# Kernel optimization log

Hardware: AMD Instinct MI355X
Metric: run time of the kernel (lower is better)

Reference implementation:

```python
import jax, jax.numpy as jnp
import numpy as np

N, E, DIN, DOUT = 10000, 160000, 256, 256
NEG_SLOPE = 0.2
BN_EPS = 1e-5
DROP_P = 0.5


def setup_inputs() -> dict:
    key = jax.random.key(0)
    ks = jax.random.split(key, 12)
    s = 1.0 / np.sqrt(DIN)
    return {
        "x": jax.random.normal(ks[0], (N, DIN), jnp.float32),
        "edge_index": jax.random.randint(ks[1], (2, E), 0, N, jnp.int64),
        "Wl": jax.random.normal(ks[2], (DIN, DOUT), jnp.float32) * s,
        "bl": jax.random.normal(ks[3], (DOUT,), jnp.float32) * s,
        "Wr": jax.random.normal(ks[4], (DIN, DOUT), jnp.float32) * s,
        "br": jax.random.normal(ks[5], (DOUT,), jnp.float32) * s,
        "att": jax.random.normal(ks[6], (DOUT,), jnp.float32) * (1.0 / np.sqrt(DOUT)),
        "bias": jax.random.normal(ks[7], (DOUT,), jnp.float32) * 0.01,
        "gamma": jnp.ones((DOUT,), jnp.float32),
        "beta": jnp.zeros((DOUT,), jnp.float32),
        "dropout_u": jax.random.uniform(ks[8], (N, DOUT), jnp.float32),
    }


def reference(x, edge_index, Wl, bl, Wr, br, att, bias, gamma, beta, dropout_u):
    n = x.shape[0]
    # GATv2Conv (heads=1): separate source/target linear maps
    xl = x @ Wl + bl  # source features [N, DOUT]
    xr = x @ Wr + br  # target features [N, DOUT]
    # add self-loops (PyG default add_self_loops=True)
    loop = jnp.arange(n, dtype=edge_index.dtype)
    src = jnp.concatenate([edge_index[0], loop])  # [E+N]
    dst = jnp.concatenate([edge_index[1], loop])
    # GATv2 attention: e = att . LeakyReLU(xl_j + xr_i)
    h = jax.nn.leaky_relu(xl[src] + xr[dst], NEG_SLOPE)  # [E+N, DOUT]
    alpha = h @ att  # [E+N]
    # segment softmax over destination nodes
    amax = jax.ops.segment_max(alpha, dst, num_segments=n)
    alpha = jnp.exp(alpha - amax[dst])
    denom = jax.ops.segment_sum(alpha, dst, num_segments=n)
    alpha = alpha / denom[dst]
    # scatter-add aggregate of weighted source features
    out = jax.ops.segment_sum(xl[src] * alpha[:, None], dst, num_segments=n)
    out = out + bias
    # ReLU -> dropout(p=0.5, training) -> BatchNorm (training stats)
    out = jax.nn.relu(out)
    mask = (dropout_u >= DROP_P).astype(out.dtype) / (1.0 - DROP_P)
    out = out * mask
    mean = out.mean(axis=0)
    var = out.var(axis=0)  # biased, as BatchNorm uses for normalization
    out = gamma * (out - mean) * jax.lax.rsqrt(var + BN_EPS) + beta
    return out
```

## Files before the change

kernel.cpp:

```cpp
#include <hip/hip_runtime.h>
#include <hip/hip_bf16.h>
#include <math.h>

#define D 256
#define CAP 128
#define NEG_SLOPE 0.2f
#define BN_EPS 1e-5f
#define NBKT 64

typedef __attribute__((ext_vector_type(8))) short bf16x8;
typedef __attribute__((ext_vector_type(8))) unsigned short ushort8;
typedef __attribute__((ext_vector_type(4))) unsigned short ushort4v;
typedef __attribute__((ext_vector_type(4))) float f32x4;

__device__ inline unsigned short f2bf(float f) {
    union { float f; unsigned u; } v; v.f = f;
    unsigned u = v.u;
    unsigned r = u + 0x7FFFu + ((u >> 16) & 1u);
    return (unsigned short)(r >> 16);
}
__device__ inline float bf2f(unsigned short u) {
    union { unsigned u; float f; } v; v.u = ((unsigned)u) << 16; return v.f;
}

__device__ __forceinline__ void gload16(const void* g, void* l) {
    __builtin_amdgcn_global_load_lds(
        (const __attribute__((address_space(1))) unsigned int*)g,
        (__attribute__((address_space(3))) unsigned int*)l,
        16, 0, 0);
}

__global__ void prep_kernel(const float* __restrict__ X,
                            const float* __restrict__ Wl, const float* __restrict__ Wr,
                            int* __restrict__ zero_base, int nzero, int nzb,
                            unsigned short* __restrict__ Bt,
                            unsigned short* __restrict__ Xbf, int N) {
    int b = blockIdx.x;
    if (b < nzb) {
        int idx = b * 256 + threadIdx.x;
        if (idx < nzero) zero_base[idx] = 0;
    } else if (b < nzb + 128) {
        __shared__ float tile[32][33];
        int b2 = b - nzb;
        const float* W = (b2 < 64) ? Wl : Wr;
        int nbase = (b2 < 64) ? 0 : 256;
        int t2 = b2 & 63;
        int ti = t2 >> 3;
        int tj = t2 & 7;
        int t = threadIdx.x;
        int r = t >> 3;
        int c4 = (t & 7) * 4;
        float4 v = *(const float4*)(W + (size_t)(ti * 32 + r) * 256 + tj * 32 + c4);
        tile[r][c4] = v.x; tile[r][c4 + 1] = v.y;
        tile[r][c4 + 2] = v.z; tile[r][c4 + 3] = v.w;
        __syncthreads();
        int nl = t >> 3;
        int n = tj * 32 + nl;
        int k0 = ti * 32 + c4;
        int ks = k0 ^ ((n & 7) << 3);
        ushort4v o;
        o[0] = f2bf(tile[c4][nl]);
        o[1] = f2bf(tile[c4 + 1][nl]);
        o[2] = f2bf(tile[c4 + 2][nl]);
        o[3] = f2bf(tile[c4 + 3][nl]);
        *(ushort4v*)(Bt + (size_t)(nbase + n) * 256 + ks) = o;
    } else {
        int idx = (b - nzb - 128) * 256 + threadIdx.x;
        int row = idx >> 5;
        int k0 = (idx & 31) * 8;
        int ks = k0 ^ ((row & 7) << 3);
        ushort8 v = {0, 0, 0, 0, 0, 0, 0, 0};
        if (row < N) {
            const float* src = X + (size_t)row * 256 + k0;
            float4 f0 = *(const float4*)(src);
            float4 f1 = *(const float4*)(src + 4);
            v[0] = f2bf(f0.x); v[1] = f2bf(f0.y);
            v[2] = f2bf(f0.z); v[3] = f2bf(f0.w);
            v[4] = f2bf(f1.x); v[5] = f2bf(f1.y);
            v[6] = f2bf(f1.z); v[7] = f2bf(f1.w);
        }
        *(ushort8*)(Xbf + (size_t)row * 256 + ks) = v;
    }
}

__global__ __launch_bounds__(256) void gemm_scatter_kernel(
    const unsigned short* __restrict__ Xbf, const unsigned short* __restrict__ Bt,
    const float* __restrict__ bl, const float* __restrict__ br,
    const int* __restrict__ ei, int* __restrict__ counts, int* __restrict__ ssrc,
    unsigned short* __restrict__ xlbf, unsigned short* __restrict__ xrbf,
    int M, int E, int N, int ngemm, int nMtiles)
{
    if ((int)blockIdx.x >= ngemm) {
        int e = (blockIdx.x - ngemm) * 256 + threadIdx.x;
        if (e < E + N) {
            int src, dst;
            if (e < E) { src = ei[e]; dst = ei[E + e]; }
            else       { src = dst = e - E; }
            int pos = atomicAdd(&counts[dst], 1);
            if (pos < CAP) ssrc[dst * CAP + pos] = src;
        }
        return;
    }

    const int b = blockIdx.x;
    const int r = (b & 7) + 8 * (b >> 6);
    const int c = (b >> 3) & 7;
    if (r >= nMtiles) return;

    __shared__ __align__(16) unsigned short As[64 * 128];
    __shared__ __align__(16) unsigned short Bs[64 * 128];

    const int tid = threadIdx.x;
    const int wave = tid >> 6, lane = tid & 63;
    const int m_l = lane & 15, quad = lane >> 4;
    const int row0 = r * 64;
    const int n0 = c * 64;
    const int sw = (m_l & 7) << 3;

    f32x4 acc[4] = {};

    for (int k0 = 0; k0 < 256; k0 += 128) {
        __syncthreads();
        #pragma unroll
        for (int i = 0; i < 4; i++) {
            int L = (tid + i * 256) * 16;
            int rr = L >> 8;
            int cb = L & 255;
            gload16((const char*)Xbf + (size_t)(row0 + rr) * 512 + (size_t)k0 * 2 + cb,
                    (char*)As + L);
            gload16((const char*)Bt + (size_t)(n0 + rr) * 512 + (size_t)k0 * 2 + cb,
                    (char*)Bs + L);
        }
        __syncthreads();

        #pragma unroll
        for (int kk0 = 0; kk0 < 128; kk0 += 32) {
            int ka = (kk0 + quad * 8) ^ sw;
            bf16x8 a = *(const bf16x8*)&As[(wave * 16 + m_l) * 128 + ka];
            #pragma unroll
            for (int cc = 0; cc < 4; cc++) {
                bf16x8 bv = *(const bf16x8*)&Bs[(cc * 16 + m_l) * 128 + ka];
                acc[cc] = __builtin_amdgcn_mfma_f32_16x16x32_bf16(a, bv, acc[cc], 0, 0, 0);
            }
        }
    }

    const bool isl = (n0 < 256);
    #pragma unroll
    for (int cc = 0; cc < 4; cc++) {
        int col = n0 + cc * 16 + m_l;
        int col8 = col & 255;
        float bv = isl ? bl[col8] : br[col8];
        #pragma unroll
        for (int rr = 0; rr < 4; rr++) {
            int row = row0 + wave * 16 + quad * 4 + rr;
            if (row < M) {
                float v = acc[cc][rr] + bv;
                if (isl) xlbf[(size_t)row * 256 + col8] = f2bf(v);
                else     xrbf[(size_t)row * 256 + col8] = f2bf(v);
            }
        }
    }
}

__device__ __forceinline__ float dot8leakyc(ushort8 c, float4 bA, float4 bB,
                                            float4 aA, float4 aB) {
    float h, s = 0.f;
    h = bf2f(c[0]) + bA.x; h = (h > 0.f) ? h : NEG_SLOPE * h; s += h * aA.x;
    h = bf2f(c[1]) + bA.y; h = (h > 0.f) ? h : NEG_SLOPE * h; s += h * aA.y;
    h = bf2f(c[2]) + bA.z; h = (h > 0.f) ? h : NEG_SLOPE * h; s += h * aA.z;
    h = bf2f(c[3]) + bA.w; h = (h > 0.f) ? h : NEG_SLOPE * h; s += h * aA.w;
    h = bf2f(c[4]) + bB.x; h = (h > 0.f) ? h : NEG_SLOPE * h; s += h * aB.x;
    h = bf2f(c[5]) + bB.y; h = (h > 0.f) ? h : NEG_SLOPE * h; s += h * aB.y;
    h = bf2f(c[6]) + bB.z; h = (h > 0.f) ? h : NEG_SLOPE * h; s += h * aB.z;
    h = bf2f(c[7]) + bB.w; h = (h > 0.f) ? h : NEG_SLOPE * h; s += h * aB.w;
    return s;
}

__global__ __launch_bounds__(256, 4) void node_kernel(
    const unsigned short* __restrict__ xlbf, const unsigned short* __restrict__ xrbf,
    const float* __restrict__ att, const float* __restrict__ bias,
    const float* __restrict__ du, const int* __restrict__ counts,
    const int* __restrict__ ssrc, float* __restrict__ out,
    float* __restrict__ bsum, float* __restrict__ bsq, int N)
{
    __shared__ float ls[4][256];

    const int wave = threadIdx.x >> 6, lane = threadIdx.x & 63;
    const int i = blockIdx.x * 4 + wave;
    const bool valid = (i < N);
    const int hl = lane & 31;
    const int sid = lane >> 5;

    int cnt = valid ? counts[i] : 0;
    if (cnt > CAP) cnt = CAP;
    const int start = i * CAP, end = start + cnt;

    const ushort8 z8 = {0, 0, 0, 0, 0, 0, 0, 0};
    const float4 attA = ((const float4*)att)[hl * 2];
    const float4 attB = ((const float4*)att)[hl * 2 + 1];
    ushort8 xrv = valid ? *(const ushort8*)(xrbf + (size_t)i * D + hl * 8) : z8;
    float4 bA, bB;
    bA.x = bf2f(xrv[0]); bA.y = bf2f(xrv[1]); bA.z = bf2f(xrv[2]); bA.w = bf2f(xrv[3]);
    bB.x = bf2f(xrv[4]); bB.y = bf2f(xrv[5]); bB.z = bf2f(xrv[6]); bB.w = bf2f(xrv[7]);

    float lsum = 0.f;
    float acc[8] = {0.f, 0.f, 0.f, 0.f, 0.f, 0.f, 0.f, 0.f};
    const unsigned short* xb = xlbf + hl * 8;

    for (int cs = start; cs < end; cs += 64) {
        const int cend = (end < cs + 64) ? end : cs + 64;
        int srcv = ssrc[cs + lane];
        int e = cs + sid;

        ushort8 p0, p1, p2, p3;
        {
            int a0 = __shfl(srcv, sid);
            int a1 = __shfl(srcv, sid + 2);
            int a2 = __shfl(srcv, sid + 4);
            int a3 = __shfl(srcv, sid + 6);
            p0 = (e     < cend) ? *(const ushort8*)(xb + (size_t)a0 * D) : z8;
            p1 = (e + 2 < cend) ? *(const ushort8*)(xb + (size_t)a1 * D) : z8;
            p2 = (e + 4 < cend) ? *(const ushort8*)(xb + (size_t)a2 * D) : z8;
            p3 = (e + 6 < cend) ? *(const ushort8*)(xb + (size_t)a3 * D) : z8;
        }

        while (e < cend) {
            ushort8 c0 = p0, c1 = p1, c2 = p2, c3 = p3;
            bool v1 = (e + 2 < cend), v2 = (e + 4 < cend), v3 = (e + 6 < cend);
            int en = e + 8;
            {
                int on = (en - cs) & 63;
                int a0 = __shfl(srcv, on);
                int a1 = __shfl(srcv, on + 2);
                int a2 = __shfl(srcv, on + 4);
                int a3 = __shfl(srcv, on + 6);
                p0 = (en     < cend) ? *(const ushort8*)(xb + (size_t)a0 * D) : z8;
                p1 = (en + 2 < cend) ? *(const ushort8*)(xb + (size_t)a1 * D) : z8;
                p2 = (en + 4 < cend) ? *(const ushort8*)(xb + (size_t)a2 * D) : z8;
                p3 = (en + 6 < cend) ? *(const ushort8*)(xb + (size_t)a3 * D) : z8;
            }

            float s0 = dot8leakyc(c0, bA, bB, attA, attB);
            float s1 = dot8leakyc(c1, bA, bB, attA, attB);
            float s2 = dot8leakyc(c2, bA, bB, attA, attB);
            float s3 = dot8leakyc(c3, bA, bB, attA, attB);

            #pragma unroll
            for (int off = 1; off < 32; off <<= 1) {
                s0 += __shfl_xor(s0, off);
                s1 += __shfl_xor(s1, off);
                s2 += __shfl_xor(s2, off);
                s3 += __shfl_xor(s3, off);
            }
            if (!v1) s1 = -INFINITY;
            if (!v2) s2 = -INFINITY;
            if (!v3) s3 = -INFINITY;

            float e0e = __expf(s0);
            float e1e = __expf(s1);
            float e2e = __expf(s2);
            float e3e = __expf(s3);
            lsum += e0e + e1e + e2e + e3e;
            #pragma unroll
            for (int k = 0; k < 8; k++) {
                acc[k] += e0e * bf2f(c0[k]) + e1e * bf2f(c1[k])
                        + e2e * bf2f(c2[k]) + e3e * bf2f(c3[k]);
            }
            e = en;
        }
    }

    float4 uA, uB;
    if (valid && lane < 32) {
        uA = ((const float4*)(du + (size_t)i * D))[hl * 2];
        uB = ((const float4*)(du + (size_t)i * D))[hl * 2 + 1];
    }

    lsum += __shfl_xor(lsum, 32);
    #pragma unroll
    for (int k = 0; k < 8; k++) acc[k] += __shfl_xor(acc[k], 32);

    float ov[8];
    if (lane < 32) {
        if (valid) {
            float inv = 1.f / lsum;
            float4 biA = ((const float4*)bias)[hl * 2];
            float4 biB = ((const float4*)bias)[hl * 2 + 1];
            float4 oA, oB;
            oA.x = fmaxf(acc[0] * inv + biA.x, 0.f); oA.x = (uA.x >= 0.5f) ? 2.f * oA.x : 0.f;
            oA.y = fmaxf(acc[1] * inv + biA.y, 0.f); oA.y = (uA.y >= 0.5f) ? 2.f * oA.y : 0.f;
            oA.z = fmaxf(acc[2] * inv + biA.z, 0.f); oA.z = (uA.z >= 0.5f) ? 2.f * oA.z : 0.f;
            oA.w = fmaxf(acc[3] * inv + biA.w, 0.f); oA.w = (uA.w >= 0.5f) ? 2.f * oA.w : 0.f;
            oB.x = fmaxf(acc[4] * inv + biB.x, 0.f); oB.x = (uB.x >= 0.5f) ? 2.f * oB.x : 0.f;
            oB.y = fmaxf(acc[5] * inv + biB.y, 0.f); oB.y = (uB.y >= 0.5f) ? 2.f * oB.y : 0.f;
            oB.z = fmaxf(acc[6] * inv + biB.z, 0.f); oB.z = (uB.z >= 0.5f) ? 2.f * oB.z : 0.f;
            oB.w = fmaxf(acc[7] * inv + biB.w, 0.f); oB.w = (uB.w >= 0.5f) ? 2.f * oB.w : 0.f;
            ((float4*)(out + (size_t)i * D))[hl * 2] = oA;
            ((float4*)(out + (size_t)i * D))[hl * 2 + 1] = oB;
            ov[0] = oA.x; ov[1] = oA.y; ov[2] = oA.z; ov[3] = oA.w;
            ov[4] = oB.x; ov[5] = oB.y; ov[6] = oB.z; ov[7] = oB.w;
        } else {
            #pragma unroll
            for (int k = 0; k < 8; k++) ov[k] = 0.f;
        }
        #pragma unroll
        for (int k = 0; k < 8; k++) ls[wave][hl * 8 + k] = ov[k];
    }
    __syncthreads();

    {
        int t = threadIdx.x;
        float s = 0.f, s2 = 0.f;
        #pragma unroll
        for (int w = 0; w < 4; w++) {
            float v = ls[w][t];
            s += v; s2 += v * v;
        }
        int bkt = (blockIdx.x & (NBKT - 1)) * 256 + t;
        atomicAdd(&bsum[bkt], s);
        atomicAdd(&bsq[bkt], s2);
    }
}

__global__ __launch_bounds__(256) void bn_apply_kernel(
    float* __restrict__ out,
    const float* __restrict__ bsum, const float* __restrict__ bsq,
    const float* __restrict__ gamma, const float* __restrict__ beta, int N)
{
    __shared__ float scaleL[256], shiftL[256];
    const int t = threadIdx.x;
    float s = 0.f, s2 = 0.f;
    #pragma unroll 8
    for (int b = 0; b < NBKT; b++) {
        s += bsum[b * 256 + t];
        s2 += bsq[b * 256 + t];
    }
    float invN = 1.f / (float)N;
    float mean = s * invN;
    float var = s2 * invN - mean * mean;
    float rs = rsqrtf(var + BN_EPS);
    float sc = gamma[t] * rs;
    scaleL[t] = sc;
    shiftL[t] = beta[t] - mean * sc;
    __syncthreads();

    const int c4 = t & 63;
    float4 scv, shv;
    scv.x = scaleL[c4 * 4];     shv.x = shiftL[c4 * 4];
    scv.y = scaleL[c4 * 4 + 1]; shv.y = shiftL[c4 * 4 + 1];
    scv.z = scaleL[c4 * 4 + 2]; shv.z = shiftL[c4 * 4 + 2];
    scv.w = scaleL[c4 * 4 + 3]; shv.w = shiftL[c4 * 4 + 3];

    for (int row = blockIdx.x * 4 + (t >> 6); row < N; row += gridDim.x * 4) {
        float4 v = ((float4*)(out + (size_t)row * D))[c4];
        v.x = v.x * scv.x + shv.x;
        v.y = v.y * scv.y + shv.y;
        v.z = v.z * scv.z + shv.z;
        v.w = v.w * scv.w + shv.w;
        ((float4*)(out + (size_t)row * D))[c4] = v;
    }
}

extern "C" void kernel_launch(void* const* d_in, const int* in_sizes, int n_in,
                              void* d_out, int out_size, void* d_ws, size_t ws_size,
                              hipStream_t stream) {
    const float* x     = (const float*)d_in[0];
    const int*   ei    = (const int*)d_in[1];
    const float* Wl    = (const float*)d_in[2];
    const float* bl    = (const float*)d_in[3];
    const float* Wr    = (const float*)d_in[4];
    const float* br    = (const float*)d_in[5];
    const float* att   = (const float*)d_in[6];
    const float* bias  = (const float*)d_in[7];
    const float* gamma = (const float*)d_in[8];
    const float* beta  = (const float*)d_in[9];
    const float* du    = (const float*)d_in[10];

    const int N = in_sizes[0] / D;
    const int E = in_sizes[1] / 2;
    const int Mpad = (N + 63) & ~63;

    int* ws = (int*)d_ws;
    size_t off = 0;
    unsigned short* xrbf = (unsigned short*)(ws + off); off += (size_t)N * D / 2;
    unsigned short* xlbf = (unsigned short*)(ws + off); off += (size_t)N * D / 2;
    unsigned short* Xbf  = (unsigned short*)(ws + off); off += (size_t)Mpad * D / 2;
    unsigned short* Bt   = (unsigned short*)(ws + off); off += 512 * 256 / 2;
    int*   ssrc     = ws + off;           off += (size_t)N * CAP;
    float* bsum     = (float*)(ws + off); off += NBKT * 256;
    float* bsq      = (float*)(ws + off); off += NBKT * 256;
    int*   counts   = ws + off;           off += N;
    int nzero = 2 * NBKT * 256 + N;
    int nzb = (nzero + 255) / 256;

    int nconv = (Mpad * 32) / 256;
    prep_kernel<<<nzb + 128 + nconv, 256, 0, stream>>>(
        x, Wl, Wr, (int*)bsum, nzero, nzb, Bt, Xbf, N);

    int nMtiles = (N + 63) / 64;
    int nMgroups = (nMtiles + 7) / 8;
    int ngemm = nMgroups * 64;
    int nscat = (E + N + 255) / 256;
    gemm_scatter_kernel<<<ngemm + nscat, 256, 0, stream>>>(
        Xbf, Bt, bl, br, ei, counts, ssrc, xlbf, xrbf, N, E, N, ngemm, nMtiles);

    node_kernel<<<(N + 3) / 4, 256, 0, stream>>>(
        xlbf, xrbf, att, bias, du, counts, ssrc, (float*)d_out, bsum, bsq, N);

    bn_apply_kernel<<<256, 256, 0, stream>>>(
        (float*)d_out, bsum, bsq, gamma, beta, N);
}
```

Before: 140.1 us.

## Use packed f32x2 math in node kernel and drop gather bounds predicates

Converts the bf16 unpack, LeakyReLU dot product and weighted accumulation in the node kernel to two-wide float vectors so the compiler can emit packed FP32 instructions, and replaces the compare-select LeakyReLU with a max. It removes the per-load validity predicates on neighbour gathers by moving ssrc after counts and zero-filling the whole ssrc buffer in the prep kernel, so out-of-range slots read row 0 safely. The aim is fewer VALU ops and branches per edge, at the cost of zeroing an extra N*CAP ints (about 5 MB) every call.

Result: no change. 138.0 us (-1.5%).

```diff
diff --git a/kernel.cpp b/kernel.cpp
--- a/kernel.cpp
+++ b/kernel.cpp
@@ -12,6 +12,7 @@
 typedef __attribute__((ext_vector_type(8))) unsigned short ushort8;
 typedef __attribute__((ext_vector_type(4))) unsigned short ushort4v;
 typedef __attribute__((ext_vector_type(4))) float f32x4;
+typedef __attribute__((ext_vector_type(2))) float f32x2;
 
 __device__ inline unsigned short f2bf(float f) {
     union { float f; unsigned u; } v; v.f = f;
@@ -21,6 +22,18 @@
 }
 __device__ inline float bf2f(unsigned short u) {
     union { unsigned u; float f; } v; v.u = ((unsigned)u) << 16; return v.f;
+}
+
+__device__ __forceinline__ void unpack8(ushort8 c, f32x2* f) {
+    const unsigned* u = (const unsigned*)&c;
+    #pragma unroll
+    for (int j = 0; j < 4; j++) {
+        union { unsigned q; float s; } lo, hi;
+        lo.q = u[j] << 16;
+        hi.q = u[j] & 0xffff0000u;
+        f32x2 v; v.x = lo.s; v.y = hi.s;
+        f[j] = v;
+    }
 }
 
 __device__ __forceinline__ void gload16(const void* g, void* l) {
@@ -163,18 +176,16 @@
     }
 }
 
-__device__ __forceinline__ float dot8leakyc(ushort8 c, float4 bA, float4 bB,
-                                            float4 aA, float4 aB) {
-    float h, s = 0.f;
-    h = bf2f(c[0]) + bA.x; h = (h > 0.f) ? h : NEG_SLOPE * h; s += h * aA.x;
-    h = bf2f(c[1]) + bA.y; h = (h > 0.f) ? h : NEG_SLOPE * h; s += h * aA.y;
-    h = bf2f(c[2]) + bA.z; h = (h > 0.f) ? h : NEG_SLOPE * h; s += h * aA.z;
-    h = bf2f(c[3]) + bA.w; h = (h > 0.f) ? h : NEG_SLOPE * h; s += h * aA.w;
-    h = bf2f(c[4]) + bB.x; h = (h > 0.f) ? h : NEG_SLOPE * h; s += h * aB.x;
-    h = bf2f(c[5]) + bB.y; h = (h > 0.f) ? h : NEG_SLOPE * h; s += h * aB.y;
-    h = bf2f(c[6]) + bB.z; h = (h > 0.f) ? h : NEG_SLOPE * h; s += h * aB.z;
-    h = bf2f(c[7]) + bB.w; h = (h > 0.f) ? h : NEG_SLOPE * h; s += h * aB.w;
-    return s;
+__device__ __forceinline__ float dot8pk(const f32x2* f, const f32x2* b2,
+                                        const f32x2* a2) {
+    f32x2 s2 = {0.f, 0.f};
+    #pragma unroll
+    for (int j = 0; j < 4; j++) {
+        f32x2 h = f[j] + b2[j];
+        f32x2 l = __builtin_elementwise_max(h, h * 0.2f);
+        s2 += l * a2[j];
+    }
+    return s2.x + s2.y;
 }
 
 __global__ __launch_bounds__(256, 4) void node_kernel(
@@ -199,13 +210,16 @@
     const ushort8 z8 = {0, 0, 0, 0, 0, 0, 0, 0};
     const float4 attA = ((const float4*)att)[hl * 2];
     const float4 attB = ((const float4*)att)[hl * 2 + 1];
+    f32x2 a2[4];
+    a2[0].x = attA.x; a2[0].y = attA.y; a2[1].x = attA.z; a2[1].y = attA.w;
+    a2[2].x = attB.x; a2[2].y = attB.y; a2[3].x = attB.z; a2[3].y = attB.w;
+
     ushort8 xrv = valid ? *(const ushort8*)(xrbf + (size_t)i * D + hl * 8) : z8;
-    float4 bA, bB;
-    bA.x = bf2f(xrv[0]); bA.y = bf2f(xrv[1]); bA.z = bf2f(xrv[2]); bA.w = bf2f(xrv[3]);
-    bB.x = bf2f(xrv[4]); bB.y = bf2f(xrv[5]); bB.z = bf2f(xrv[6]); bB.w = bf2f(xrv[7]);
+    f32x2 b2[4];
+    unpack8(xrv, b2);
 
     float lsum = 0.f;
-    float acc[8] = {0.f, 0.f, 0.f, 0.f, 0.f, 0.f, 0.f, 0.f};
+    f32x2 acc2[4] = {};
     const unsigned short* xb = xlbf + hl * 8;
 
     for (int cs = start; cs < end; cs += 64) {
@@ -217,12 +231,12 @@
         {
             int a0 = __shfl(srcv, sid);
             int a1 = __shfl(srcv, sid + 2);
-            int a2 = __shfl(srcv, sid + 4);
+            int a2i = __shfl(srcv, sid + 4);
             int a3 = __shfl(srcv, sid + 6);
-            p0 = (e     < cend) ? *(const ushort8*)(xb + (size_t)a0 * D) : z8;
-            p1 = (e + 2 < cend) ? *(const ushort8*)(xb + (size_t)a1 * D) : z8;
-            p2 = (e + 4 < cend) ? *(const ushort8*)(xb + (size_t)a2 * D) : z8;
-            p3 = (e + 6 < cend) ? *(const ushort8*)(xb + (size_t)a3 * D) : z8;
+            p0 = *(const ushort8*)(xb + (size_t)a0 * D);
+            p1 = *(const ushort8*)(xb + (size_t)a1 * D);
+            p2 = *(const ushort8*)(xb + (size_t)a2i * D);
+            p3 = *(const ushort8*)(xb + (size_t)a3 * D);
         }
 
         while (e < cend) {
@@ -233,18 +247,22 @@
                 int on = (en - cs) & 63;
                 int a0 = __shfl(srcv, on);
                 int a1 = __shfl(srcv, on + 2);
-                int a2 = __shfl(srcv, on + 4);
+                int a2i = __shfl(srcv, on + 4);
                 int a3 = __shfl(srcv, on + 6);
-                p0 = (en     < cend) ? *(const ushort8*)(xb + (size_t)a0 * D) : z8;
-                p1 = (en + 2 < cend) ? *(const ushort8*)(xb + (size_t)a1 * D) : z8;
-                p2 = (en + 4 < cend) ? *(const ushort8*)(xb + (size_t)a2 * D) : z8;
-                p3 = (en + 6 < cend) ? *(const ushort8*)(xb + (size_t)a3 * D) : z8;
+                p0 = *(const ushort8*)(xb + (size_t)a0 * D);
+                p1 = *(const ushort8*)(xb + (size_t)a1 * D);
+                p2 = *(const ushort8*)(xb + (size_t)a2i * D);
+                p3 = *(const ushort8*)(xb + (size_t)a3 * D);
             }
 
-            float s0 = dot8leakyc(c0, bA, bB, attA, attB);
-            float s1 = dot8leakyc(c1, bA, bB, attA, attB);
-            float s2 = dot8leakyc(c2, bA, bB, attA, attB);
-            float s3 = dot8leakyc(c3, bA, bB, attA, attB);
+            f32x2 f0[4], f1[4], f2[4], f3[4];
+            unpack8(c0, f0); unpack8(c1, f1);
+            unpack8(c2, f2); unpack8(c3, f3);
+
+            float s0 = dot8pk(f0, b2, a2);
+            float s1 = dot8pk(f1, b2, a2);
+            float s2 = dot8pk(f2, b2, a2);
+            float s3 = dot8pk(f3, b2, a2);
 
             #pragma unroll
             for (int off = 1; off < 32; off <<= 1) {
@@ -263,9 +281,9 @@
             float e3e = __expf(s3);
             lsum += e0e + e1e + e2e + e3e;
             #pragma unroll
-            for (int k = 0; k < 8; k++) {
-                acc[k] += e0e * bf2f(c0[k]) + e1e * bf2f(c1[k])
-                        + e2e * bf2f(c2[k]) + e3e * bf2f(c3[k]);
+            for (int j = 0; j < 4; j++) {
+                acc2[j] += e0e * f0[j] + e1e * f1[j]
+                         + e2e * f2[j] + e3e * f3[j];
             }
             e = en;
         }
@@ -279,7 +297,10 @@
 
     lsum += __shfl_xor(lsum, 32);
     #pragma unroll
-    for (int k = 0; k < 8; k++) acc[k] += __shfl_xor(acc[k], 32);
+    for (int j = 0; j < 4; j++) {
+        acc2[j][0] += __shfl_xor(acc2[j][0], 32);
+        acc2[j][1] += __shfl_xor(acc2[j][1], 32);
+    }
 
     float ov[8];
     if (lane < 32) {
@@ -288,14 +309,14 @@
             float4 biA = ((const float4*)bias)[hl * 2];
             float4 biB = ((const float4*)bias)[hl * 2 + 1];
             float4 oA, oB;
-            oA.x = fmaxf(acc[0] * inv + biA.x, 0.f); oA.x = (uA.x >= 0.5f) ? 2.f * oA.x : 0.f;
-            oA.y = fmaxf(acc[1] * inv + biA.y, 0.f); oA.y = (uA.y >= 0.5f) ? 2.f * oA.y : 0.f;
-            oA.z = fmaxf(acc[2] * inv + biA.z, 0.f); oA.z = (uA.z >= 0.5f) ? 2.f * oA.z : 0.f;
-            oA.w = fmaxf(acc[3] * inv + biA.w, 0.f); oA.w = (uA.w >= 0.5f) ? 2.f * oA.w : 0.f;
-            oB.x = fmaxf(acc[4] * inv + biB.x, 0.f); oB.x = (uB.x >= 0.5f) ? 2.f * oB.x : 0.f;
-            oB.y = fmaxf(acc[5] * inv + biB.y, 0.f); oB.y = (uB.y >= 0.5f) ? 2.f * oB.y : 0.f;
-            oB.z = fmaxf(acc[6] * inv + biB.z, 0.f); oB.z = (uB.z >= 0.5f) ? 2.f * oB.z : 0.f;
-            oB.w = fmaxf(acc[7] * inv + biB.w, 0.f); oB.w = (uB.w >= 0.5f) ? 2.f * oB.w : 0.f;
+            oA.x = fmaxf(acc2[0][0] * inv + biA.x, 0.f); oA.x = (uA.x >= 0.5f) ? 2.f * oA.x : 0.f;
+            oA.y = fmaxf(acc2[0][1] * inv + biA.y, 0.f); oA.y = (uA.y >= 0.5f) ? 2.f * oA.y : 0.f;
+            oA.z = fmaxf(acc2[1][0] * inv + biA.z, 0.f); oA.z = (uA.z >= 0.5f) ? 2.f * oA.z : 0.f;
+            oA.w = fmaxf(acc2[1][1] * inv + biA.w, 0.f); oA.w = (uA.w >= 0.5f) ? 2.f * oA.w : 0.f;
+            oB.x = fmaxf(acc2[2][0] * inv + biB.x, 0.f); oB.x = (uB.x >= 0.5f) ? 2.f * oB.x : 0.f;
+            oB.y = fmaxf(acc2[2][1] * inv + biB.y, 0.f); oB.y = (uB.y >= 0.5f) ? 2.f * oB.y : 0.f;
+            oB.z = fmaxf(acc2[3][0] * inv + biB.z, 0.f); oB.z = (uB.z >= 0.5f) ? 2.f * oB.z : 0.f;
+            oB.w = fmaxf(acc2[3][1] * inv + biB.w, 0.f); oB.w = (uB.w >= 0.5f) ? 2.f * oB.w : 0.f;
             ((float4*)(out + (size_t)i * D))[hl * 2] = oA;
             ((float4*)(out + (size_t)i * D))[hl * 2 + 1] = oB;
             ov[0] = oA.x; ov[1] = oA.y; ov[2] = oA.z; ov[3] = oA.w;
@@ -387,11 +408,11 @@
     unsigned short* xlbf = (unsigned short*)(ws + off); off += (size_t)N * D / 2;
     unsigned short* Xbf  = (unsigned short*)(ws + off); off += (size_t)Mpad * D / 2;
     unsigned short* Bt   = (unsigned short*)(ws + off); off += 512 * 256 / 2;
-    int*   ssrc     = ws + off;           off += (size_t)N * CAP;
     float* bsum     = (float*)(ws + off); off += NBKT * 256;
     float* bsq      = (float*)(ws + off); off += NBKT * 256;
     int*   counts   = ws + off;           off += N;
-    int nzero = 2 * NBKT * 256 + N;
+    int*   ssrc     = ws + off;           off += (size_t)N * CAP;
+    int nzero = 2 * NBKT * 256 + N + N * CAP;
     int nzb = (nzero + 255) / 256;
 
     int nconv = (Mpad * 32) / 256;
```
